# Optimization experiments

Hardware: AMD Instinct MI355X
Metric: run time of the kernel (lower is better)

## Reference

```python
import jax, jax.numpy as jnp
import numpy as np

G, T, D_IN, D_OUT = 8, 8192, 1024, 1024
# fixed uneven per-expert token counts summing to T (variable-size groups)
_COUNTS = np.array([512, 1536, 1024, 1024, 768, 1280, 896, 1152], dtype=np.int32)
assert _COUNTS.sum() == T


def setup_inputs() -> dict:
    key = jax.random.key(0)
    k1, k2 = jax.random.split(key)
    hidden_states = jax.random.normal(k1, (T, D_IN), dtype=jnp.float32)
    # kaiming_uniform_(a=sqrt(5)) on [G, in, out] -> bound = sqrt(3/ (fan_in)) with gain sqrt(1/3)
    bound = 1.0 / np.sqrt(D_IN)
    weight = jax.random.uniform(k2, (G, D_IN, D_OUT), dtype=jnp.float32, minval=-bound, maxval=bound)
    tokens_per_expert = jnp.asarray(_COUNTS)
    return {"hidden_states": hidden_states, "weight": weight, "tokens_per_expert": tokens_per_expert}


def reference(hidden_states, weight, tokens_per_expert):
    # grouped GEMM: token t in group g (per contiguous split by tokens_per_expert)
    # gets out[t] = hidden_states[t] @ weight[g]
    T_ = hidden_states.shape[0]
    G_ = weight.shape[0]
    offsets = jnp.cumsum(tokens_per_expert)  # [G] end offsets of each group
    expert_id = jnp.searchsorted(offsets, jnp.arange(T_), side="right")  # [T]
    out = jnp.zeros((T_, weight.shape[2]), dtype=hidden_states.dtype)
    for g in range(G_):  # small fixed expert count; masked accumulate keeps shapes static
        mask = (expert_id == g).astype(hidden_states.dtype)[:, None]
        out = out + mask * (hidden_states @ weight[g])
    return out
```

## Files before the change

### kernel.cpp

```cpp
#include <hip/hip_runtime.h>
#include <hip/hip_bf16.h>
#include <stdint.h>

typedef __attribute__((ext_vector_type(8))) short short8;
typedef __attribute__((ext_vector_type(4))) float f32x4;

constexpr int Tt = 8192, Kd = 1024, Nd = 1024, Gn = 8;
constexpr int BM = 128, BN = 128, BK = 32;
constexpr int NKT = Kd / BK;

static __device__ __forceinline__ short f2bf(float x) {
    __hip_bfloat16 b = __float2bfloat16(x);
    return *reinterpret_cast<short*>(&b);
}

__global__ __launch_bounds__(256, 3)
void grouped_gemm_kernel(const float* __restrict__ H,
                         const float* __restrict__ W,
                         const int* __restrict__ counts,
                         float* __restrict__ out)
{
    __shared__ __align__(16) float Asf[2][BM * BK];
    __shared__ __align__(16) short Bss[2][BN * BK];

    const int tid = threadIdx.x;
    const int bid = blockIdx.x;
    const int wg = (bid & 7) * 64 + (bid >> 3);
    const int mt = wg >> 3, nt = wg & 7;
    const int row0 = mt * BM, col0 = nt * BN;

    int g = 0;
    {
        int c = 0;
        for (int i = 0; i < Gn; ++i) { c += counts[i]; if (row0 >= c) g = i + 1; }
    }
    const float* __restrict__ Wg = W + (size_t)g * Kd * Nd;

    const int wid = tid >> 6, lane = tid & 63;
    const int wm = wid >> 1, wn = wid & 1;
    const int l15 = lane & 15, l4 = lane >> 4;

    f32x4 acc[4][4];
#pragma unroll
    for (int i = 0; i < 4; ++i)
#pragma unroll
        for (int j = 0; j < 4; ++j) acc[i][j] = (f32x4)0.0f;

    float breg[16];
    const int bn = tid & 127, bkh = tid >> 7;

    auto stage_a = [&](int kt, int buf) {
        const int kbase = kt * BK;
#pragma unroll
        for (int i = 0; i < 4; ++i) {
            const int q = wid * 4 + i;
            const int d = q * 64 + lane;
            const int m = d >> 3, gc = d & 7;
            const float* src = H + (size_t)(row0 + m) * Kd + kbase + ((gc ^ (m & 7)) << 2);
            __builtin_amdgcn_global_load_lds(
                (const __attribute__((address_space(1))) uint32_t*)src,
                (__attribute__((address_space(3))) uint32_t*)(&Asf[buf][q * 256]),
                16, 0, 0);
        }
    };

    auto load_b = [&](int kt) {
        const float* p = Wg + (size_t)(kt * BK + bkh * 16) * Nd + col0 + bn;
#pragma unroll
        for (int j = 0; j < 16; ++j) breg[j] = p[(size_t)j * Nd];
    };

    auto write_b = [&](int buf) {
        short8 v0, v1;
#pragma unroll
        for (int j = 0; j < 8; ++j) { v0[j] = f2bf(breg[j]); v1[j] = f2bf(breg[8 + j]); }
        const int g0 = (bkh * 2) ^ (bn & 3), g1 = (bkh * 2 + 1) ^ (bn & 3);
        *(short8*)&Bss[buf][bn * 32 + g0 * 8] = v0;
        *(short8*)&Bss[buf][bn * 32 + g1 * 8] = v1;
    };

    auto compute = [&](int buf) {
        short8 af[4], bf[4];
#pragma unroll
        for (int mi = 0; mi < 4; ++mi) {
            const int m = wm * 64 + mi * 16 + l15;
            const int s = m & 7;
            const f32x4 x0 = *(const f32x4*)&Asf[buf][m * 32 + (((l4 * 2) ^ s) << 2)];
            const f32x4 x1 = *(const f32x4*)&Asf[buf][m * 32 + (((l4 * 2 + 1) ^ s) << 2)];
            short8 v;
#pragma unroll
            for (int j = 0; j < 4; ++j) { v[j] = f2bf(x0[j]); v[4 + j] = f2bf(x1[j]); }
            af[mi] = v;
        }
#pragma unroll
        for (int ni = 0; ni < 4; ++ni) {
            const int n = wn * 64 + ni * 16 + l15;
            bf[ni] = *(const short8*)&Bss[buf][n * 32 + ((l4 ^ (n & 3)) << 3)];
        }
#pragma unroll
        for (int mi = 0; mi < 4; ++mi)
#pragma unroll
            for (int ni = 0; ni < 4; ++ni)
                acc[mi][ni] = __builtin_amdgcn_mfma_f32_16x16x32_bf16(
                    af[mi], bf[ni], acc[mi][ni], 0, 0, 0);
    };

    stage_a(0, 0);
    load_b(0);
    write_b(0);
    __syncthreads();

    int buf = 0;
    for (int kt = 0; kt < NKT; ++kt) {
        const bool more = (kt + 1 < NKT);
        if (more) { stage_a(kt + 1, buf ^ 1); load_b(kt + 1); }
        compute(buf);
        if (more) write_b(buf ^ 1);
        __syncthreads();
        buf ^= 1;
    }

#pragma unroll
    for (int mi = 0; mi < 4; ++mi) {
        const int rbase = row0 + wm * 64 + mi * 16 + l4 * 4;
#pragma unroll
        for (int ni = 0; ni < 4; ++ni) {
            const int c = col0 + wn * 64 + ni * 16 + l15;
#pragma unroll
            for (int r = 0; r < 4; ++r)
                out[(size_t)(rbase + r) * Nd + c] = acc[mi][ni][r];
        }
    }
}

extern "C" void kernel_launch(void* const* d_in, const int* in_sizes, int n_in,
                              void* d_out, int out_size, void* d_ws, size_t ws_size,
                              hipStream_t stream) {
    const float* H = (const float*)d_in[0];
    const float* W = (const float*)d_in[1];
    const int* counts = (const int*)d_in[2];
    float* out = (float*)d_out;
    const int grid = (Tt / BM) * (Nd / BN);
    grouped_gemm_kernel<<<grid, 256, 0, stream>>>(H, W, counts, out);
}
```

Before: 48.13 us.

## Enlarge tiles to 128x256x64 with 8 waves, bf16 A staging and interleaved MFMA schedule

Raises the tile to 128x256 with a K-step of 64 and 512 threads. A is now loaded through registers and converted to bf16 once before the LDS write, instead of being staged as fp32 with global_load_lds and converted in every compute pass. The main loop splits the MFMA work into quadrants with s_setprio and overlaps the LDS writes for the next stage with the MFMAs. The aim is more reuse per byte loaded and fewer redundant conversions, at the cost of higher register pressure (32 B values per thread), fewer blocks (256), and the loss of asynchronous direct-to-LDS loads for A.

```diff
diff --git a/kernel.cpp b/kernel.cpp
--- a/kernel.cpp
+++ b/kernel.cpp
@@ -6,7 +6,7 @@
 typedef __attribute__((ext_vector_type(4))) float f32x4;
 
 constexpr int Tt = 8192, Kd = 1024, Nd = 1024, Gn = 8;
-constexpr int BM = 128, BN = 128, BK = 32;
+constexpr int BM = 128, BN = 256, BK = 64;
 constexpr int NKT = Kd / BK;
 
 static __device__ __forceinline__ short f2bf(float x) {
@@ -14,19 +14,19 @@
     return *reinterpret_cast<short*>(&b);
 }
 
-__global__ __launch_bounds__(256, 3)
+__global__ __launch_bounds__(512, 2)
 void grouped_gemm_kernel(const float* __restrict__ H,
                          const float* __restrict__ W,
                          const int* __restrict__ counts,
                          float* __restrict__ out)
 {
-    __shared__ __align__(16) float Asf[2][BM * BK];
-    __shared__ __align__(16) short Bss[2][BN * BK];
+    __shared__ __align__(16) short As[2][BM * BK];
+    __shared__ __align__(16) short Bs[2][BN * BK];
 
     const int tid = threadIdx.x;
     const int bid = blockIdx.x;
-    const int wg = (bid & 7) * 64 + (bid >> 3);
-    const int mt = wg >> 3, nt = wg & 7;
+    const int swz = (bid & 7) * 32 + (bid >> 3);
+    const int mt = swz >> 2, nt = swz & 3;
     const int row0 = mt * BM, col0 = nt * BN;
 
     int g = 0;
@@ -37,8 +37,11 @@
     const float* __restrict__ Wg = W + (size_t)g * Kd * Nd;
 
     const int wid = tid >> 6, lane = tid & 63;
-    const int wm = wid >> 1, wn = wid & 1;
+    const int wm = wid >> 2, wn = wid & 3;
     const int l15 = lane & 15, l4 = lane >> 4;
+
+    const int ra = tid >> 2, ca = tid & 3;
+    const int nb = tid & 255, kh = tid >> 8;
 
     f32x4 acc[4][4];
 #pragma unroll
@@ -46,77 +49,122 @@
 #pragma unroll
         for (int j = 0; j < 4; ++j) acc[i][j] = (f32x4)0.0f;
 
-    float breg[16];
-    const int bn = tid & 127, bkh = tid >> 7;
+    f32x4 av[4];
+    float bv[32];
 
-    auto stage_a = [&](int kt, int buf) {
-        const int kbase = kt * BK;
+    auto load_a = [&](int kt) {
+        const float* p = H + (size_t)(row0 + ra) * Kd + kt * BK + ca * 16;
 #pragma unroll
-        for (int i = 0; i < 4; ++i) {
-            const int q = wid * 4 + i;
-            const int d = q * 64 + lane;
-            const int m = d >> 3, gc = d & 7;
-            const float* src = H + (size_t)(row0 + m) * Kd + kbase + ((gc ^ (m & 7)) << 2);
-            __builtin_amdgcn_global_load_lds(
-                (const __attribute__((address_space(1))) uint32_t*)src,
-                (__attribute__((address_space(3))) uint32_t*)(&Asf[buf][q * 256]),
-                16, 0, 0);
+        for (int j = 0; j < 4; ++j) av[j] = *(const f32x4*)(p + j * 4);
+    };
+    auto load_b = [&](int kt) {
+        const float* p = Wg + (size_t)(kt * BK + kh * 32) * Nd + col0 + nb;
+#pragma unroll
+        for (int j = 0; j < 32; ++j) bv[j] = p[(size_t)j * Nd];
+    };
+    auto write_a = [&](int buf) {
+        short8 v0, v1;
+#pragma unroll
+        for (int j = 0; j < 4; ++j) {
+            v0[j] = f2bf(av[0][j]); v0[4 + j] = f2bf(av[1][j]);
+            v1[j] = f2bf(av[2][j]); v1[4 + j] = f2bf(av[3][j]);
+        }
+        const int s = ra & 7;
+        *(short8*)&As[buf][ra * 64 + (((ca * 2) ^ s) << 3)] = v0;
+        *(short8*)&As[buf][ra * 64 + (((ca * 2 + 1) ^ s) << 3)] = v1;
+    };
+    auto write_b = [&](int buf) {
+        const int s = nb & 7;
+#pragma unroll
+        for (int c = 0; c < 4; ++c) {
+            short8 v;
+#pragma unroll
+            for (int j = 0; j < 8; ++j) v[j] = f2bf(bv[c * 8 + j]);
+            *(short8*)&Bs[buf][nb * 64 + (((kh * 4 + c) ^ s) << 3)] = v;
         }
     };
 
-    auto load_b = [&](int kt) {
-        const float* p = Wg + (size_t)(kt * BK + bkh * 16) * Nd + col0 + bn;
-#pragma unroll
-        for (int j = 0; j < 16; ++j) breg[j] = p[(size_t)j * Nd];
+    auto rd_a = [&](int buf, int mi, int ks) -> short8 {
+        const int m = wm * 64 + mi * 16 + l15;
+        return *(const short8*)&As[buf][m * 64 + (((ks * 4 + l4) ^ (m & 7)) << 3)];
+    };
+    auto rd_b = [&](int buf, int ni, int ks) -> short8 {
+        const int n = wn * 64 + ni * 16 + l15;
+        return *(const short8*)&Bs[buf][n * 64 + (((ks * 4 + l4) ^ (n & 7)) << 3)];
     };
 
-    auto write_b = [&](int buf) {
-        short8 v0, v1;
-#pragma unroll
-        for (int j = 0; j < 8; ++j) { v0[j] = f2bf(breg[j]); v1[j] = f2bf(breg[8 + j]); }
-        const int g0 = (bkh * 2) ^ (bn & 3), g1 = (bkh * 2 + 1) ^ (bn & 3);
-        *(short8*)&Bss[buf][bn * 32 + g0 * 8] = v0;
-        *(short8*)&Bss[buf][bn * 32 + g1 * 8] = v1;
-    };
-
-    auto compute = [&](int buf) {
-        short8 af[4], bf[4];
-#pragma unroll
-        for (int mi = 0; mi < 4; ++mi) {
-            const int m = wm * 64 + mi * 16 + l15;
-            const int s = m & 7;
-            const f32x4 x0 = *(const f32x4*)&Asf[buf][m * 32 + (((l4 * 2) ^ s) << 2)];
-            const f32x4 x1 = *(const f32x4*)&Asf[buf][m * 32 + (((l4 * 2 + 1) ^ s) << 2)];
-            short8 v;
-#pragma unroll
-            for (int j = 0; j < 4; ++j) { v[j] = f2bf(x0[j]); v[4 + j] = f2bf(x1[j]); }
-            af[mi] = v;
-        }
-#pragma unroll
-        for (int ni = 0; ni < 4; ++ni) {
-            const int n = wn * 64 + ni * 16 + l15;
-            bf[ni] = *(const short8*)&Bss[buf][n * 32 + ((l4 ^ (n & 3)) << 3)];
-        }
-#pragma unroll
-        for (int mi = 0; mi < 4; ++mi)
-#pragma unroll
-            for (int ni = 0; ni < 4; ++ni)
-                acc[mi][ni] = __builtin_amdgcn_mfma_f32_16x16x32_bf16(
-                    af[mi], bf[ni], acc[mi][ni], 0, 0, 0);
-    };
-
-    stage_a(0, 0);
-    load_b(0);
-    write_b(0);
-    __syncthreads();
+    load_a(0); load_b(0);
+    write_a(0); write_b(0);
+    asm volatile("s_waitcnt lgkmcnt(0)" ::: "memory");
+    __builtin_amdgcn_s_barrier();
 
     int buf = 0;
     for (int kt = 0; kt < NKT; ++kt) {
         const bool more = (kt + 1 < NKT);
-        if (more) { stage_a(kt + 1, buf ^ 1); load_b(kt + 1); }
-        compute(buf);
-        if (more) write_b(buf ^ 1);
-        __syncthreads();
+        if (more) { load_a(kt + 1); load_b(kt + 1); }
+
+        short8 a0[2][2], a1[2][2], b0[2][2], b1[2][2];
+
+#pragma unroll
+        for (int i = 0; i < 2; ++i)
+#pragma unroll
+            for (int ks = 0; ks < 2; ++ks) { a0[i][ks] = rd_a(buf, i, ks); b0[i][ks] = rd_b(buf, i, ks); }
+        __builtin_amdgcn_s_setprio(1);
+#pragma unroll
+        for (int mi = 0; mi < 2; ++mi)
+#pragma unroll
+            for (int ni = 0; ni < 2; ++ni)
+#pragma unroll
+                for (int ks = 0; ks < 2; ++ks)
+                    acc[mi][ni] = __builtin_amdgcn_mfma_f32_16x16x32_bf16(
+                        a0[mi][ks], b0[ni][ks], acc[mi][ni], 0, 0, 0);
+        __builtin_amdgcn_s_setprio(0);
+
+#pragma unroll
+        for (int i = 0; i < 2; ++i)
+#pragma unroll
+            for (int ks = 0; ks < 2; ++ks) a1[i][ks] = rd_a(buf, 2 + i, ks);
+        __builtin_amdgcn_s_setprio(1);
+#pragma unroll
+        for (int mi = 0; mi < 2; ++mi)
+#pragma unroll
+            for (int ni = 0; ni < 2; ++ni)
+#pragma unroll
+                for (int ks = 0; ks < 2; ++ks)
+                    acc[2 + mi][ni] = __builtin_amdgcn_mfma_f32_16x16x32_bf16(
+                        a1[mi][ks], b0[ni][ks], acc[2 + mi][ni], 0, 0, 0);
+        __builtin_amdgcn_s_setprio(0);
+
+        if (more) { write_a(buf ^ 1); write_b(buf ^ 1); }
+
+#pragma unroll
+        for (int i = 0; i < 2; ++i)
+#pragma unroll
+            for (int ks = 0; ks < 2; ++ks) b1[i][ks] = rd_b(buf, 2 + i, ks);
+        __builtin_amdgcn_s_setprio(1);
+#pragma unroll
+        for (int mi = 0; mi < 2; ++mi)
+#pragma unroll
+            for (int ni = 0; ni < 2; ++ni)
+#pragma unroll
+                for (int ks = 0; ks < 2; ++ks)
+                    acc[2 + mi][2 + ni] = __builtin_amdgcn_mfma_f32_16x16x32_bf16(
+                        a1[mi][ks], b1[ni][ks], acc[2 + mi][2 + ni], 0, 0, 0);
+        __builtin_amdgcn_s_setprio(0);
+
+        __builtin_amdgcn_s_setprio(1);
+#pragma unroll
+        for (int mi = 0; mi < 2; ++mi)
+#pragma unroll
+            for (int ni = 0; ni < 2; ++ni)
+#pragma unroll
+                for (int ks = 0; ks < 2; ++ks)
+                    acc[mi][2 + ni] = __builtin_amdgcn_mfma_f32_16x16x32_bf16(
+                        a0[mi][ks], b1[ni][ks], acc[mi][2 + ni], 0, 0, 0);
+        __builtin_amdgcn_s_setprio(0);
+
+        asm volatile("s_waitcnt lgkmcnt(0)" ::: "memory");
+        __builtin_amdgcn_s_barrier();
         buf ^= 1;
     }
 
@@ -141,5 +189,5 @@
     const int* counts = (const int*)d_in[2];
     float* out = (float*)d_out;
     const int grid = (Tt / BM) * (Nd / BN);
-    grouped_gemm_kernel<<<grid, 256, 0, stream>>>(H, W, counts, out);
+    grouped_gemm_kernel<<<grid, 512, 0, stream>>>(H, W, counts, out);
 }
```

Result: faster. 39.22 us (-18.5%).

## Convert A to bf16 before LDS and prefetch B two K-tiles ahead

Applied to the files above, without the earlier changes.

A tiles are now loaded into registers, converted to bf16 once and stored to LDS as bf16, replacing the fp32 global-to-LDS DMA path that re-converted A in every compute step. B gets two register buffers so its global loads run two K-tiles ahead, and the loop is unrolled by two with a lighter barrier that only waits on LDS counters. The cost is higher register pressure (launch bounds lowered to 2 blocks per SM) and losing the async direct-to-LDS load for A.

```diff
diff --git a/kernel.cpp b/kernel.cpp
--- a/kernel.cpp
+++ b/kernel.cpp
@@ -14,14 +14,30 @@
     return *reinterpret_cast<short*>(&b);
 }
 
-__global__ __launch_bounds__(256, 3)
-void grouped_gemm_kernel(const float* __restrict__ H,
-                         const float* __restrict__ W,
-                         const int* __restrict__ counts,
-                         float* __restrict__ out)
+#define BAR() do { \
+    asm volatile("s_waitcnt lgkmcnt(0)" ::: "memory"); \
+    __builtin_amdgcn_s_barrier(); \
+    __builtin_amdgcn_sched_barrier(0); \
+} while (0)
+
+#define LOAD_B(dst, kt) do { \
+    const float* p = Wg + (size_t)((kt) * BK + kh * 16) * Nd + col0 + rr; \
+    _Pragma("unroll") for (int j = 0; j < 16; ++j) dst[j] = p[(size_t)j * Nd]; \
+} while (0)
+
+#define WRITE_B(src, buf) do { \
+    short8 v0, v1; \
+    _Pragma("unroll") for (int j = 0; j < 8; ++j) { v0[j] = f2bf(src[j]); v1[j] = f2bf(src[8 + j]); } \
+    *(short8*)&Bs[buf][rr * 32 + (((kh * 2) ^ xr) << 3)] = v0; \
+    *(short8*)&Bs[buf][rr * 32 + (((kh * 2 + 1) ^ xr) << 3)] = v1; \
+} while (0)
+
+__global__ __launch_bounds__(256, 2)
+void gemm_fused(const float* __restrict__ H, const float* __restrict__ W,
+                const int* __restrict__ counts, float* __restrict__ out)
 {
-    __shared__ __align__(16) float Asf[2][BM * BK];
-    __shared__ __align__(16) short Bss[2][BN * BK];
+    __shared__ __align__(16) short As[2][BM * BK];
+    __shared__ __align__(16) short Bs[2][BN * BK];
 
     const int tid = threadIdx.x;
     const int bid = blockIdx.x;
@@ -30,15 +46,17 @@
     const int row0 = mt * BM, col0 = nt * BN;
 
     int g = 0;
-    {
-        int c = 0;
-        for (int i = 0; i < Gn; ++i) { c += counts[i]; if (row0 >= c) g = i + 1; }
-    }
+    { int c = 0; for (int i = 0; i < Gn; ++i) { c += counts[i]; if (row0 >= c) g = i + 1; } }
     const float* __restrict__ Wg = W + (size_t)g * Kd * Nd;
 
     const int wid = tid >> 6, lane = tid & 63;
     const int wm = wid >> 1, wn = wid & 1;
     const int l15 = lane & 15, l4 = lane >> 4;
+    const int xl = (l15 ^ (l15 >> 2)) & 3;
+
+    const int rr = tid >> 1;
+    const int kh = tid & 1;
+    const int xr = (rr ^ (rr >> 2)) & 3;
 
     f32x4 acc[4][4];
 #pragma unroll
@@ -46,37 +64,21 @@
 #pragma unroll
         for (int j = 0; j < 4; ++j) acc[i][j] = (f32x4)0.0f;
 
-    float breg[16];
-    const int bn = tid & 127, bkh = tid >> 7;
+    f32x4 av[4];
+    float bv0[16], bv1[16];
 
-    auto stage_a = [&](int kt, int buf) {
-        const int kbase = kt * BK;
+    auto load_a = [&](int kt) {
+        const float* p = H + (size_t)(row0 + rr) * Kd + kt * BK + kh * 16;
 #pragma unroll
-        for (int i = 0; i < 4; ++i) {
-            const int q = wid * 4 + i;
-            const int d = q * 64 + lane;
-            const int m = d >> 3, gc = d & 7;
-            const float* src = H + (size_t)(row0 + m) * Kd + kbase + ((gc ^ (m & 7)) << 2);
-            __builtin_amdgcn_global_load_lds(
-                (const __attribute__((address_space(1))) uint32_t*)src,
-                (__attribute__((address_space(3))) uint32_t*)(&Asf[buf][q * 256]),
-                16, 0, 0);
-        }
+        for (int j = 0; j < 4; ++j) av[j] = *(const f32x4*)(p + j * 4);
     };
-
-    auto load_b = [&](int kt) {
-        const float* p = Wg + (size_t)(kt * BK + bkh * 16) * Nd + col0 + bn;
-#pragma unroll
-        for (int j = 0; j < 16; ++j) breg[j] = p[(size_t)j * Nd];
-    };
-
-    auto write_b = [&](int buf) {
+    auto write_a = [&](int buf) {
         short8 v0, v1;
 #pragma unroll
-        for (int j = 0; j < 8; ++j) { v0[j] = f2bf(breg[j]); v1[j] = f2bf(breg[8 + j]); }
-        const int g0 = (bkh * 2) ^ (bn & 3), g1 = (bkh * 2 + 1) ^ (bn & 3);
-        *(short8*)&Bss[buf][bn * 32 + g0 * 8] = v0;
-        *(short8*)&Bss[buf][bn * 32 + g1 * 8] = v1;
+        for (int j = 0; j < 4; ++j) { v0[j] = f2bf(av[0][j]); v0[4 + j] = f2bf(av[1][j]);
+                                      v1[j] = f2bf(av[2][j]); v1[4 + j] = f2bf(av[3][j]); }
+        *(short8*)&As[buf][rr * 32 + (((kh * 2) ^ xr) << 3)] = v0;
+        *(short8*)&As[buf][rr * 32 + (((kh * 2 + 1) ^ xr) << 3)] = v1;
     };
 
     auto compute = [&](int buf) {
@@ -84,18 +86,12 @@
 #pragma unroll
         for (int mi = 0; mi < 4; ++mi) {
             const int m = wm * 64 + mi * 16 + l15;
-            const int s = m & 7;
-            const f32x4 x0 = *(const f32x4*)&Asf[buf][m * 32 + (((l4 * 2) ^ s) << 2)];
-            const f32x4 x1 = *(const f32x4*)&Asf[buf][m * 32 + (((l4 * 2 + 1) ^ s) << 2)];
-            short8 v;
-#pragma unroll
-            for (int j = 0; j < 4; ++j) { v[j] = f2bf(x0[j]); v[4 + j] = f2bf(x1[j]); }
-            af[mi] = v;
+            af[mi] = *(const short8*)&As[buf][m * 32 + ((l4 ^ xl) << 3)];
         }
 #pragma unroll
         for (int ni = 0; ni < 4; ++ni) {
             const int n = wn * 64 + ni * 16 + l15;
-            bf[ni] = *(const short8*)&Bss[buf][n * 32 + ((l4 ^ (n & 3)) << 3)];
+            bf[ni] = *(const short8*)&Bs[buf][n * 32 + ((l4 ^ xl) << 3)];
         }
 #pragma unroll
         for (int mi = 0; mi < 4; ++mi)
@@ -105,19 +101,24 @@
                     af[mi], bf[ni], acc[mi][ni], 0, 0, 0);
     };
 
-    stage_a(0, 0);
-    load_b(0);
-    write_b(0);
-    __syncthreads();
+    LOAD_B(bv0, 0);
+    load_a(0);
+    WRITE_B(bv0, 0);
+    write_a(0);
+    LOAD_B(bv1, 1);
+    BAR();
 
-    int buf = 0;
-    for (int kt = 0; kt < NKT; ++kt) {
-        const bool more = (kt + 1 < NKT);
-        if (more) { stage_a(kt + 1, buf ^ 1); load_b(kt + 1); }
-        compute(buf);
-        if (more) write_b(buf ^ 1);
-        __syncthreads();
-        buf ^= 1;
+    for (int kt2 = 0; kt2 < NKT; kt2 += 2) {
+        if (kt2 + 1 < NKT) load_a(kt2 + 1);
+        if (kt2 + 2 < NKT) LOAD_B(bv0, kt2 + 2);
+        compute(0);
+        if (kt2 + 1 < NKT) { WRITE_B(bv1, 1); write_a(1); }
+        BAR();
+        if (kt2 + 2 < NKT) load_a(kt2 + 2);
+        if (kt2 + 3 < NKT) LOAD_B(bv1, kt2 + 3);
+        compute(1);
+        if (kt2 + 2 < NKT) { WRITE_B(bv0, 0); write_a(0); }
+        BAR();
     }
 
 #pragma unroll
@@ -141,5 +142,5 @@
     const int* counts = (const int*)d_in[2];
     float* out = (float*)d_out;
     const int grid = (Tt / BM) * (Nd / BN);
-    grouped_gemm_kernel<<<grid, 256, 0, stream>>>(H, W, counts, out);
+    gemm_fused<<<grid, 256, 0, stream>>>(H, W, counts, out);
 }
```

After: 62.60 us. 1.3x slower.
